# Kernel optimization log

Measured on AMD Instinct MI355X. Metric: run time of the kernel, lower is better.

## Reference

```python
import jax, jax.numpy as jnp
import numpy as np

B_TRUE, S, HEADS, DIM_HEAD, DIM, N = 2, 2, 8, 64, 512, 1024
BS = B_TRUE * S            # effective batch = (b s)
DIM_INNER = HEADS * DIM_HEAD
ALL_HEADS = S * HEADS
EPS = 1e-5


def setup_inputs() -> dict:
    key = jax.random.key(0)
    ks = jax.random.split(key, 8)
    inv = 0.02
    x = jax.random.normal(ks[0], (BS, N, DIM), dtype=jnp.float32)
    mask = jax.random.randint(ks[1], (BS, N), 0, 2).astype(bool)
    gamma = jnp.ones((DIM,), dtype=jnp.float32)
    w_qkv = jax.random.normal(ks[2], (3 * DIM_INNER, DIM), dtype=jnp.float32) * inv
    w_gates = jax.random.normal(ks[3], (HEADS, DIM), dtype=jnp.float32) * inv
    b_gates = jnp.zeros((HEADS,), dtype=jnp.float32)
    w_pre = jax.random.normal(ks[4], (ALL_HEADS, ALL_HEADS), dtype=jnp.float32) * 0.25
    w_post = jax.random.normal(ks[5], (ALL_HEADS, ALL_HEADS), dtype=jnp.float32) * 0.25
    w_out = jax.random.normal(ks[6], (DIM, DIM_INNER), dtype=jnp.float32) * inv
    return {"x": x, "mask": mask, "gamma": gamma, "w_qkv": w_qkv,
            "w_gates": w_gates, "b_gates": b_gates, "w_pre": w_pre,
            "w_post": w_post, "w_out": w_out}


def _rmsnorm(x, gamma):
    # einn.Norm('b... [d]', mean=False, bias=False): RMSNorm over last dim
    var = jnp.mean(jnp.square(x), axis=-1, keepdims=True)
    return x * jax.lax.rsqrt(var + EPS) * gamma


def reference(x, mask, gamma, w_qkv, w_gates, b_gates, w_pre, w_post, w_out):
    bs, n, dim = x.shape
    b = bs // S
    x = _rmsnorm(x, gamma)

    # QKV: 'b n (qkv h d) -> qkv b h n d'
    qkv = jnp.einsum('bnd,ed->bne', x, w_qkv)
    qkv = qkv.reshape(bs, n, 3, HEADS, DIM_HEAD).transpose(2, 0, 3, 1, 4)
    q, k, v = qkv[0], qkv[1], qkv[2]
    q = q * (DIM_HEAD ** 0.5)  # NOTE: source MULTIPLIES by sqrt(dim_head)

    sim = jnp.einsum('bhid,bhjd->bhij', q, k)  # [bs, h, n, n]
    mask_value = -jnp.finfo(sim.dtype).max

    # pre talking-heads: 1x1 conv across (s h) channels
    sim = sim.reshape(b, ALL_HEADS, n, n)
    sim = jnp.einsum('oi,binm->bonm', w_pre, sim).reshape(bs, HEADS, n, n)

    # padding mask over keys j
    sim = jnp.where(mask[:, None, None, :], sim, mask_value)

    # causal mask
    causal = jnp.triu(jnp.ones((n, n), dtype=bool), 1)
    sim = jnp.where(causal, mask_value, sim)

    attn = jax.nn.softmax(sim, axis=-1)
    post_softmax_attn = attn

    # post talking-heads
    attn = attn.reshape(b, ALL_HEADS, n, n)
    attn = jnp.einsum('oi,binm->bonm', w_post, attn).reshape(bs, HEADS, n, n)

    out = jnp.einsum('bhij,bhjd->bhid', attn, v)  # [bs, h, n, d]

    # sigmoid gates from normed x: 'b n h -> b h n 1'
    gates = jax.nn.sigmoid(jnp.einsum('bnd,hd->bnh', x, w_gates) + b_gates)
    out = out * gates.transpose(0, 2, 1)[..., None]

    # 'b h n d -> b n (h d)' then Linear(dim_inner, dim, bias=False)
    out = out.transpose(0, 2, 1, 3).reshape(bs, n, DIM_INNER)
    out = jnp.einsum('bne,de->bnd', out, w_out)
    return (out, post_softmax_attn)
```

## Files before the change

kernel.cpp:

```cpp
#include <hip/hip_runtime.h>
#include <cfloat>
#include <math.h>

#define B2   2
#define BS4  4
#define NH   8
#define DH   64
#define DIM  512
#define NSEQ 1024
#define AH   16

typedef __attribute__((ext_vector_type(8))) short short8;
typedef __attribute__((ext_vector_type(4))) float floatx4;

__device__ inline unsigned short f2bf(float x) {
    unsigned int u = __float_as_uint(x);
    unsigned int r = (u + 0x7fffu + ((u >> 16) & 1u)) >> 16;
    return (unsigned short)r;
}
__device__ inline float bf2f(unsigned short h) {
    return __uint_as_float(((unsigned int)h) << 16);
}
__device__ inline void split2(float x, unsigned short& h, unsigned short& l) {
    h = f2bf(x);
    l = f2bf(x - bf2f(h));
}

template<int MT, int NT_, bool SPLIT>
__device__ inline void mfma_nt_core(
    const unsigned short* __restrict__ Ah, const unsigned short* __restrict__ Al,
    const unsigned short* __restrict__ Bh, const unsigned short* __restrict__ Bl,
    int K, int lda, int ldb, int arow, int bcol, floatx4 acc[MT][NT_])
{
    int lane = threadIdx.x & 63;
    int lr = lane & 15, lq = lane >> 4;
    for (int k0 = 0; k0 < K; k0 += 32) {
        short8 ah[MT], al[MT], bh[NT_], bl[NT_];
        #pragma unroll
        for (int mi = 0; mi < MT; ++mi) {
            size_t off = (size_t)(arow + mi * 16 + lr) * lda + k0 + lq * 8;
            ah[mi] = *(const short8*)(Ah + off);
            if (SPLIT) al[mi] = *(const short8*)(Al + off);
        }
        #pragma unroll
        for (int ni = 0; ni < NT_; ++ni) {
            size_t off = (size_t)(bcol + ni * 16 + lr) * ldb + k0 + lq * 8;
            bh[ni] = *(const short8*)(Bh + off);
            if (SPLIT) bl[ni] = *(const short8*)(Bl + off);
        }
        #pragma unroll
        for (int mi = 0; mi < MT; ++mi)
            #pragma unroll
            for (int ni = 0; ni < NT_; ++ni) {
                acc[mi][ni] = __builtin_amdgcn_mfma_f32_16x16x32_bf16(ah[mi], bh[ni], acc[mi][ni], 0, 0, 0);
                if (SPLIT) {
                    acc[mi][ni] = __builtin_amdgcn_mfma_f32_16x16x32_bf16(ah[mi], bl[ni], acc[mi][ni], 0, 0, 0);
                    acc[mi][ni] = __builtin_amdgcn_mfma_f32_16x16x32_bf16(al[mi], bh[ni], acc[mi][ni], 0, 0, 0);
                }
            }
    }
}

__global__ __launch_bounds__(256) void k_rmsnorm_gates(
    const float* __restrict__ x, const float* __restrict__ gamma,
    const float* __restrict__ wg, const float* __restrict__ bg,
    unsigned short* __restrict__ xn_h, unsigned short* __restrict__ xn_l,
    float* __restrict__ gates)
{
    int r = blockIdx.x;
    int tid = threadIdx.x;
    const float* xr = x + (size_t)r * DIM;
    float v0 = xr[tid];
    float v1 = xr[tid + 256];
    float ss = v0 * v0 + v1 * v1;
    #pragma unroll
    for (int off = 32; off > 0; off >>= 1) ss += __shfl_down(ss, off, 64);
    __shared__ float sc[4];
    __shared__ float scw[NH][4];
    if ((tid & 63) == 0) sc[tid >> 6] = ss;
    __syncthreads();
    float tot = sc[0] + sc[1] + sc[2] + sc[3];
    float rs = rsqrtf(tot * (1.0f / DIM) + 1e-5f);
    float n0 = v0 * rs * gamma[tid];
    float n1 = v1 * rs * gamma[tid + 256];
    unsigned short hh, ll;
    split2(n0, hh, ll);
    xn_h[(size_t)r * DIM + tid] = hh; xn_l[(size_t)r * DIM + tid] = ll;
    split2(n1, hh, ll);
    xn_h[(size_t)r * DIM + tid + 256] = hh; xn_l[(size_t)r * DIM + tid + 256] = ll;
    #pragma unroll
    for (int h = 0; h < NH; ++h) {
        float p = n0 * wg[h * DIM + tid] + n1 * wg[h * DIM + tid + 256];
        #pragma unroll
        for (int off = 32; off > 0; off >>= 1) p += __shfl_down(p, off, 64);
        if ((tid & 63) == 0) scw[h][tid >> 6] = p;
    }
    __syncthreads();
    if (tid < NH) {
        float g = scw[tid][0] + scw[tid][1] + scw[tid][2] + scw[tid][3] + bg[tid];
        gates[(size_t)r * NH + tid] = 1.0f / (1.0f + __expf(-g));
    }
}

#define NQKV (3 * DIM * NH * DH)
#define NOUT (DIM * NH * DH)
__global__ __launch_bounds__(256) void k_cvt(
    const float* __restrict__ wqkv, const float* __restrict__ wout,
    unsigned short* __restrict__ wq_h, unsigned short* __restrict__ wq_l,
    unsigned short* __restrict__ wout_b)
{
    for (int i = blockIdx.x * 256 + threadIdx.x; i < NQKV + NOUT; i += gridDim.x * 256) {
        if (i < NQKV) {
            unsigned short hh, ll;
            split2(wqkv[i], hh, ll);
            wq_h[i] = hh; wq_l[i] = ll;
        } else {
            wout_b[i - NQKV] = f2bf(wout[i - NQKV]);
        }
    }
}

__global__ __launch_bounds__(256) void k_qkv_mfma(
    const unsigned short* __restrict__ xn_h, const unsigned short* __restrict__ xn_l,
    const unsigned short* __restrict__ wq_h, const unsigned short* __restrict__ wq_l,
    unsigned short* __restrict__ q_h, unsigned short* __restrict__ q_l,
    unsigned short* __restrict__ k_h, unsigned short* __restrict__ k_l,
    unsigned short* __restrict__ vT_b)
{
    int w = threadIdx.x >> 6;
    int am = blockIdx.y * 128 + (w & 1) * 64;
    int bn = blockIdx.x * 64 + (w >> 1) * 32;
    floatx4 acc[4][2];
    #pragma unroll
    for (int mi = 0; mi < 4; ++mi)
        #pragma unroll
        for (int ni = 0; ni < 2; ++ni) acc[mi][ni] = (floatx4){0.f, 0.f, 0.f, 0.f};
    mfma_nt_core<4, 2, true>(xn_h, xn_l, wq_h, wq_l, DIM, DIM, DIM, am, bn, acc);
    int lane = threadIdx.x & 63, lr = lane & 15, lq = lane >> 4;
    #pragma unroll
    for (int mi = 0; mi < 4; ++mi)
        #pragma unroll
        for (int ni = 0; ni < 2; ++ni)
            #pragma unroll
            for (int r = 0; r < 4; ++r) {
                int row = am + mi * 16 + lq * 4 + r;
                int col = bn + ni * 16 + lr;
                float v = acc[mi][ni][r];
                int bs = row >> 10, npos = row & 1023;
                int which = col >> 9, h = (col >> 6) & 7, d = col & 63;
                int bh = bs * 8 + h;
                if (which == 0) {
                    v *= 8.0f;
                    size_t idx = ((size_t)bh * NSEQ + npos) * DH + d;
                    unsigned short hh, ll; split2(v, hh, ll);
                    q_h[idx] = hh; q_l[idx] = ll;
                } else if (which == 1) {
                    size_t idx = ((size_t)bh * NSEQ + npos) * DH + d;
                    unsigned short hh, ll; split2(v, hh, ll);
                    k_h[idx] = hh; k_l[idx] = ll;
                } else {
                    vT_b[((size_t)bh * DH + d) * NSEQ + npos] = f2bf(v);
                }
            }
}

__global__ __launch_bounds__(256) void k_qk_mfma(
    const unsigned short* __restrict__ q_h, const unsigned short* __restrict__ q_l,
    const unsigned short* __restrict__ k_h, const unsigned short* __restrict__ k_l,
    float* __restrict__ simio)
{
    int bh = blockIdx.z;
    int w = threadIdx.x >> 6;
    int am = blockIdx.y * 128 + (w & 1) * 64;
    int bn = blockIdx.x * 64 + (w >> 1) * 32;
    const unsigned short* Ah = q_h + (size_t)bh * NSEQ * DH;
    const unsigned short* Al = q_l + (size_t)bh * NSEQ * DH;
    const unsigned short* Bh = k_h + (size_t)bh * NSEQ * DH;
    const unsigned short* Bl = k_l + (size_t)bh * NSEQ * DH;
    floatx4 acc[4][2];
    #pragma unroll
    for (int mi = 0; mi < 4; ++mi)
        #pragma unroll
        for (int ni = 0; ni < 2; ++ni) acc[mi][ni] = (floatx4){0.f, 0.f, 0.f, 0.f};
    mfma_nt_core<4, 2, true>(Ah, Al, Bh, Bl, DH, DH, DH, am, bn, acc);
    float* C = simio + ((size_t)bh << 20);
    int lane = threadIdx.x & 63, lr = lane & 15, lq = lane >> 4;
    #pragma unroll
    for (int mi = 0; mi < 4; ++mi)
        #pragma unroll
        for (int ni = 0; ni < 2; ++ni)
            #pragma unroll
            for (int r = 0; r < 4; ++r) {
                int row = am + mi * 16 + lq * 4 + r;
                int col = bn + ni * 16 + lr;
                C[(size_t)row * NSEQ + col] = acc[mi][ni][r];
            }
}

__global__ __launch_bounds__(256) void k_talk_softmax(
    float* __restrict__ simio, const int* __restrict__ mask,
    const float* __restrict__ wpre, const float* __restrict__ wpost,
    unsigned short* __restrict__ attn2_b)
{
    const int i = blockIdx.x;
    const int b = blockIdx.y;
    const int tid = threadIdx.x;
    const int wid = tid >> 6, lane = tid & 63;
    const int j0 = tid << 2;
    const size_t cstride = (size_t)NSEQ * NSEQ;
    const size_t rbase = (size_t)(b * 16) * cstride + (size_t)i * NSEQ + j0;

    const int4 mi0 = *(const int4*)(mask + (size_t)(b * 2 + 0) * NSEQ + j0);
    const int4 mi1 = *(const int4*)(mask + (size_t)(b * 2 + 1) * NSEQ + j0);
    bool mb[2][4];
    mb[0][0] = (mi0.x != 0) && (j0 + 0 <= i);
    mb[0][1] = (mi0.y != 0) && (j0 + 1 <= i);
    mb[0][2] = (mi0.z != 0) && (j0 + 2 <= i);
    mb[0][3] = (mi0.w != 0) && (j0 + 3 <= i);
    mb[1][0] = (mi1.x != 0) && (j0 + 0 <= i);
    mb[1][1] = (mi1.y != 0) && (j0 + 1 <= i);
    mb[1][2] = (mi1.z != 0) && (j0 + 2 <= i);
    mb[1][3] = (mi1.w != 0) && (j0 + 3 <= i);

    float val[16][4];
    #pragma unroll
    for (int o = 0; o < 16; ++o) {
        val[o][0] = 0.f; val[o][1] = 0.f; val[o][2] = 0.f; val[o][3] = 0.f;
    }
    #pragma unroll
    for (int c = 0; c < 16; ++c) {
        float4 r = *(const float4*)(simio + rbase + (size_t)c * cstride);
        #pragma unroll
        for (int o = 0; o < 16; ++o) {
            float w = wpre[o * 16 + c];
            val[o][0] = fmaf(w, r.x, val[o][0]);
            val[o][1] = fmaf(w, r.y, val[o][1]);
            val[o][2] = fmaf(w, r.z, val[o][2]);
            val[o][3] = fmaf(w, r.w, val[o][3]);
        }
    }
    #pragma unroll
    for (int o = 0; o < 16; ++o) {
        const int s = o >> 3;
        #pragma unroll
        for (int u = 0; u < 4; ++u)
            if (!mb[s][u]) val[o][u] = -FLT_MAX;
    }

    __shared__ float red[16][4];
    __shared__ float finmx[16];
    __shared__ float fininv[16];

    #pragma unroll
    for (int o = 0; o < 16; ++o) {
        float m = fmaxf(fmaxf(val[o][0], val[o][1]), fmaxf(val[o][2], val[o][3]));
        #pragma unroll
        for (int off = 32; off > 0; off >>= 1) m = fmaxf(m, __shfl_xor(m, off, 64));
        if (lane == 0) red[o][wid] = m;
    }
    __syncthreads();
    if (tid < 16)
        finmx[tid] = fmaxf(fmaxf(red[tid][0], red[tid][1]), fmaxf(red[tid][2], red[tid][3]));
    __syncthreads();

    #pragma unroll
    for (int o = 0; o < 16; ++o) {
        float mx = finmx[o];
        val[o][0] = __expf(val[o][0] - mx);
        val[o][1] = __expf(val[o][1] - mx);
        val[o][2] = __expf(val[o][2] - mx);
        val[o][3] = __expf(val[o][3] - mx);
        float s = (val[o][0] + val[o][1]) + (val[o][2] + val[o][3]);
        #pragma unroll
        for (int off = 32; off > 0; off >>= 1) s += __shfl_xor(s, off, 64);
        if (lane == 0) red[o][wid] = s;
    }
    __syncthreads();
    if (tid < 16)
        fininv[tid] = 1.0f / (red[tid][0] + red[tid][1] + red[tid][2] + red[tid][3]);
    __syncthreads();

    #pragma unroll
    for (int o = 0; o < 16; ++o) {
        float inv = fininv[o];
        val[o][0] *= inv; val[o][1] *= inv; val[o][2] *= inv; val[o][3] *= inv;
        *(float4*)(simio + rbase + (size_t)o * cstride) =
            make_float4(val[o][0], val[o][1], val[o][2], val[o][3]);
    }

    #pragma unroll
    for (int o = 0; o < 16; ++o) {
        float a0 = 0.f, a1 = 0.f, a2 = 0.f, a3 = 0.f;
        #pragma unroll
        for (int c = 0; c < 16; ++c) {
            float w = wpost[o * 16 + c];
            a0 = fmaf(w, val[c][0], a0);
            a1 = fmaf(w, val[c][1], a1);
            a2 = fmaf(w, val[c][2], a2);
            a3 = fmaf(w, val[c][3], a3);
        }
        unsigned long long pk = (unsigned long long)f2bf(a0)
                              | ((unsigned long long)f2bf(a1) << 16)
                              | ((unsigned long long)f2bf(a2) << 32)
                              | ((unsigned long long)f2bf(a3) << 48);
        *(unsigned long long*)(attn2_b + rbase + (size_t)o * cstride) = pk;
    }
}

__global__ __launch_bounds__(256) void k_av_mfma(
    const unsigned short* __restrict__ attn2_b, const unsigned short* __restrict__ vT_b,
    const float* __restrict__ gates, unsigned short* __restrict__ gated_b)
{
    int bh = blockIdx.y;
    int bs = bh >> 3, h = bh & 7;
    int w = threadIdx.x >> 6;
    int am = blockIdx.x * 64 + (w & 1) * 32;
    int bn = (w >> 1) * 32;
    const unsigned short* Ah = attn2_b + ((size_t)bh << 20);
    const unsigned short* Bh = vT_b + (size_t)bh * DH * NSEQ;
    floatx4 acc[2][2];
    #pragma unroll
    for (int mi = 0; mi < 2; ++mi)
        #pragma unroll
        for (int ni = 0; ni < 2; ++ni) acc[mi][ni] = (floatx4){0.f, 0.f, 0.f, 0.f};
    mfma_nt_core<2, 2, false>(Ah, nullptr, Bh, nullptr, NSEQ, NSEQ, NSEQ, am, bn, acc);
    int lane = threadIdx.x & 63, lr = lane & 15, lq = lane >> 4;
    #pragma unroll
    for (int mi = 0; mi < 2; ++mi)
        #pragma unroll
        for (int ni = 0; ni < 2; ++ni)
            #pragma unroll
            for (int r = 0; r < 4; ++r) {
                int i = am + mi * 16 + lq * 4 + r;
                int d = bn + ni * 16 + lr;
                float g = gates[((size_t)bs * NSEQ + i) * NH + h];
                gated_b[((size_t)bs * NSEQ + i) * DIM + h * DH + d] = f2bf(acc[mi][ni][r] * g);
            }
}

__global__ __launch_bounds__(256) void k_out_mfma(
    const unsigned short* __restrict__ gated_b, const unsigned short* __restrict__ wout_b,
    float* __restrict__ out)
{
    int w = threadIdx.x >> 6;
    int am = blockIdx.y * 64 + (w & 1) * 32;
    int bn = blockIdx.x * 64 + (w >> 1) * 32;
    floatx4 acc[2][2];
    #pragma unroll
    for (int mi = 0; mi < 2; ++mi)
        #pragma unroll
        for (int ni = 0; ni < 2; ++ni) acc[mi][ni] = (floatx4){0.f, 0.f, 0.f, 0.f};
    mfma_nt_core<2, 2, false>(gated_b, nullptr, wout_b, nullptr, DIM, DIM, DIM, am, bn, acc);
    int lane = threadIdx.x & 63, lr = lane & 15, lq = lane >> 4;
    #pragma unroll
    for (int mi = 0; mi < 2; ++mi)
        #pragma unroll
        for (int ni = 0; ni < 2; ++ni)
            #pragma unroll
            for (int r = 0; r < 4; ++r) {
                int row = am + mi * 16 + lq * 4 + r;
                int col = bn + ni * 16 + lr;
                out[(size_t)row * DIM + col] = acc[mi][ni][r];
            }
}

extern "C" void kernel_launch(void* const* d_in, const int* in_sizes, int n_in,
                              void* d_out, int out_size, void* d_ws, size_t ws_size,
                              hipStream_t stream)
{
    (void)in_sizes; (void)n_in; (void)out_size; (void)ws_size;

    const float* x     = (const float*)d_in[0];
    const int*   mask  = (const int*)  d_in[1];
    const float* gamma = (const float*)d_in[2];
    const float* wqkv  = (const float*)d_in[3];
    const float* wg    = (const float*)d_in[4];
    const float* bg    = (const float*)d_in[5];
    const float* wpre  = (const float*)d_in[6];
    const float* wpost = (const float*)d_in[7];
    const float* wout  = (const float*)d_in[8];

    float* out      = (float*)d_out;
    float* attn_out = out + (size_t)BS4 * NSEQ * DIM;

    char* ws = (char*)d_ws;
    unsigned short* xn_h    = (unsigned short*)(ws);
    unsigned short* xn_l    = (unsigned short*)(ws + 4194304);
    unsigned short* wq_h    = (unsigned short*)(ws + 8388608);
    unsigned short* wq_l    = (unsigned short*)(ws + 9961472);
    unsigned short* wout_b  = (unsigned short*)(ws + 11534336);
    float*          gates   = (float*)         (ws + 12058624);
    unsigned short* q_h     = (unsigned short*)(ws + 12189696);
    unsigned short* q_l     = (unsigned short*)(ws + 16384000);
    unsigned short* k_h     = (unsigned short*)(ws + 20578304);
    unsigned short* k_l     = (unsigned short*)(ws + 24772608);
    unsigned short* vT_b    = (unsigned short*)(ws + 28966912);
    unsigned short* gated_b = (unsigned short*)(ws + 33161216);
    unsigned short* attn2_b = (unsigned short*)(ws + 37355520);

    k_rmsnorm_gates<<<dim3(BS4 * NSEQ), dim3(256), 0, stream>>>(x, gamma, wg, bg, xn_h, xn_l, gates);
    k_cvt<<<dim3(1024), dim3(256), 0, stream>>>(wqkv, wout, wq_h, wq_l, wout_b);
    k_qkv_mfma<<<dim3(24, 32), dim3(256), 0, stream>>>(xn_h, xn_l, wq_h, wq_l, q_h, q_l, k_h, k_l, vT_b);
    k_qk_mfma<<<dim3(16, 8, 32), dim3(256), 0, stream>>>(q_h, q_l, k_h, k_l, attn_out);
    k_talk_softmax<<<dim3(NSEQ, B2), dim3(256), 0, stream>>>(attn_out, mask, wpre, wpost, attn2_b);
    k_av_mfma<<<dim3(16, 32), dim3(256), 0, stream>>>(attn2_b, vT_b, gates, gated_b);
    k_out_mfma<<<dim3(8, 64), dim3(256), 0, stream>>>(gated_b, wout_b, out);
}
```

Measured before the change: 409.9 us.

## Split talking-heads softmax into separate stats and normalize kernels

Splits the fused talking-heads softmax into two kernels. A reduce kernel computes per-row max and inverse sum and writes them to scratch. A norm kernel recomputes the pre-mix, normalizes, writes probabilities with nontemporal stores, and applies the post-mix. This removes the block-level reductions and barriers from the writing kernel, but re-reads the full similarity tensor and adds one launch.

```diff
diff --git a/kernel.cpp b/kernel.cpp
--- a/kernel.cpp
+++ b/kernel.cpp
@@ -197,10 +197,10 @@
             }
 }
 
-__global__ __launch_bounds__(256) void k_talk_softmax(
-    float* __restrict__ simio, const int* __restrict__ mask,
-    const float* __restrict__ wpre, const float* __restrict__ wpost,
-    unsigned short* __restrict__ attn2_b)
+__global__ __launch_bounds__(256) void k_talk_reduce(
+    const float* __restrict__ simio, const int* __restrict__ mask,
+    const float* __restrict__ wpre,
+    float* __restrict__ mx_out, float* __restrict__ inv_out)
 {
     const int i = blockIdx.x;
     const int b = blockIdx.y;
@@ -249,7 +249,6 @@
 
     __shared__ float red[16][4];
     __shared__ float finmx[16];
-    __shared__ float fininv[16];
 
     #pragma unroll
     for (int o = 0; o < 16; ++o) {
@@ -266,26 +265,81 @@
     #pragma unroll
     for (int o = 0; o < 16; ++o) {
         float mx = finmx[o];
-        val[o][0] = __expf(val[o][0] - mx);
-        val[o][1] = __expf(val[o][1] - mx);
-        val[o][2] = __expf(val[o][2] - mx);
-        val[o][3] = __expf(val[o][3] - mx);
-        float s = (val[o][0] + val[o][1]) + (val[o][2] + val[o][3]);
+        float s = (__expf(val[o][0] - mx) + __expf(val[o][1] - mx))
+                + (__expf(val[o][2] - mx) + __expf(val[o][3] - mx));
         #pragma unroll
         for (int off = 32; off > 0; off >>= 1) s += __shfl_xor(s, off, 64);
         if (lane == 0) red[o][wid] = s;
     }
     __syncthreads();
-    if (tid < 16)
-        fininv[tid] = 1.0f / (red[tid][0] + red[tid][1] + red[tid][2] + red[tid][3]);
-    __syncthreads();
-
-    #pragma unroll
-    for (int o = 0; o < 16; ++o) {
-        float inv = fininv[o];
-        val[o][0] *= inv; val[o][1] *= inv; val[o][2] *= inv; val[o][3] *= inv;
-        *(float4*)(simio + rbase + (size_t)o * cstride) =
-            make_float4(val[o][0], val[o][1], val[o][2], val[o][3]);
+    if (tid < 16) {
+        size_t sidx = ((size_t)b * NSEQ + i) * 16 + tid;
+        mx_out[sidx] = finmx[tid];
+        inv_out[sidx] = 1.0f / (red[tid][0] + red[tid][1] + red[tid][2] + red[tid][3]);
+    }
+}
+
+__global__ __launch_bounds__(256) void k_talk_norm(
+    float* __restrict__ simio, const int* __restrict__ mask,
+    const float* __restrict__ wpre, const float* __restrict__ wpost,
+    const float* __restrict__ mx_in, const float* __restrict__ inv_in,
+    unsigned short* __restrict__ attn2_b)
+{
+    const int i = blockIdx.x;
+    const int b = blockIdx.y;
+    const int tid = threadIdx.x;
+    const int j0 = tid << 2;
+    const size_t cstride = (size_t)NSEQ * NSEQ;
+    const size_t rbase = (size_t)(b * 16) * cstride + (size_t)i * NSEQ + j0;
+
+    const int4 mi0 = *(const int4*)(mask + (size_t)(b * 2 + 0) * NSEQ + j0);
+    const int4 mi1 = *(const int4*)(mask + (size_t)(b * 2 + 1) * NSEQ + j0);
+    bool mb[2][4];
+    mb[0][0] = (mi0.x != 0) && (j0 + 0 <= i);
+    mb[0][1] = (mi0.y != 0) && (j0 + 1 <= i);
+    mb[0][2] = (mi0.z != 0) && (j0 + 2 <= i);
+    mb[0][3] = (mi0.w != 0) && (j0 + 3 <= i);
+    mb[1][0] = (mi1.x != 0) && (j0 + 0 <= i);
+    mb[1][1] = (mi1.y != 0) && (j0 + 1 <= i);
+    mb[1][2] = (mi1.z != 0) && (j0 + 2 <= i);
+    mb[1][3] = (mi1.w != 0) && (j0 + 3 <= i);
+
+    float val[16][4];
+    #pragma unroll
+    for (int o = 0; o < 16; ++o) {
+        val[o][0] = 0.f; val[o][1] = 0.f; val[o][2] = 0.f; val[o][3] = 0.f;
+    }
+    #pragma unroll
+    for (int c = 0; c < 16; ++c) {
+        float4 r = *(const float4*)(simio + rbase + (size_t)c * cstride);
+        #pragma unroll
+        for (int o = 0; o < 16; ++o) {
+            float w = wpre[o * 16 + c];
+            val[o][0] = fmaf(w, r.x, val[o][0]);
+            val[o][1] = fmaf(w, r.y, val[o][1]);
+            val[o][2] = fmaf(w, r.z, val[o][2]);
+            val[o][3] = fmaf(w, r.w, val[o][3]);
+        }
+    }
+    #pragma unroll
+    for (int o = 0; o < 16; ++o) {
+        const int s = o >> 3;
+        #pragma unroll
+        for (int u = 0; u < 4; ++u)
+            if (!mb[s][u]) val[o][u] = -FLT_MAX;
+    }
+
+    const size_t sidx = ((size_t)b * NSEQ + i) * 16;
+    #pragma unroll
+    for (int o = 0; o < 16; ++o) {
+        float mx = mx_in[sidx + o];
+        float inv = inv_in[sidx + o];
+        val[o][0] = __expf(val[o][0] - mx) * inv;
+        val[o][1] = __expf(val[o][1] - mx) * inv;
+        val[o][2] = __expf(val[o][2] - mx) * inv;
+        val[o][3] = __expf(val[o][3] - mx) * inv;
+        floatx4 st = {val[o][0], val[o][1], val[o][2], val[o][3]};
+        __builtin_nontemporal_store(st, (floatx4*)(simio + rbase + (size_t)o * cstride));
     }
 
     #pragma unroll
@@ -398,11 +452,15 @@
     unsigned short* gated_b = (unsigned short*)(ws + 33161216);
     unsigned short* attn2_b = (unsigned short*)(ws + 37355520);
 
+    float* mx_stats  = (float*)xn_h;
+    float* inv_stats = (float*)xn_l;
+
     k_rmsnorm_gates<<<dim3(BS4 * NSEQ), dim3(256), 0, stream>>>(x, gamma, wg, bg, xn_h, xn_l, gates);
     k_cvt<<<dim3(1024), dim3(256), 0, stream>>>(wqkv, wout, wq_h, wq_l, wout_b);
     k_qkv_mfma<<<dim3(24, 32), dim3(256), 0, stream>>>(xn_h, xn_l, wq_h, wq_l, q_h, q_l, k_h, k_l, vT_b);
     k_qk_mfma<<<dim3(16, 8, 32), dim3(256), 0, stream>>>(q_h, q_l, k_h, k_l, attn_out);
-    k_talk_softmax<<<dim3(NSEQ, B2), dim3(256), 0, stream>>>(attn_out, mask, wpre, wpost, attn2_b);
+    k_talk_reduce<<<dim3(NSEQ, B2), dim3(256), 0, stream>>>(attn_out, mask, wpre, mx_stats, inv_stats);
+    k_talk_norm<<<dim3(NSEQ, B2), dim3(256), 0, stream>>>(attn_out, mask, wpre, wpost, mx_stats, inv_stats, attn2_b);
     k_av_mfma<<<dim3(16, 32), dim3(256), 0, stream>>>(attn2_b, vT_b, gates, gated_b);
     k_out_mfma<<<dim3(8, 64), dim3(256), 0, stream>>>(gated_b, wout_b, out);
 }
```

After: 462.5 us. +12.8%, slower.

## Store raw scores in row-interleaved workspace and stream probabilities with nontemporal stores

Applied to the files above, without the earlier changes.

The QK kernel now writes raw scores into a workspace laid out as [b][row][channel][col], so each talking-heads block reads its 16 channels from one contiguous 64KB region instead of 16 strided 4MB planes. Post-softmax probabilities go straight to the output with nontemporal stores. The post-mixed bf16 attention is written in place over the same workspace row, and the AV kernel reads it with a 32768-element row stride. The aim is better locality and fewer cache conflicts in the softmax kernel. The cost is a larger fp32 workspace and a strided A-operand in AV, which relies on the bf16 write never overtaking unread fp32 data in the same row.

```diff
diff --git a/kernel.cpp b/kernel.cpp
--- a/kernel.cpp
+++ b/kernel.cpp
@@ -167,9 +167,11 @@
 __global__ __launch_bounds__(256) void k_qk_mfma(
     const unsigned short* __restrict__ q_h, const unsigned short* __restrict__ q_l,
     const unsigned short* __restrict__ k_h, const unsigned short* __restrict__ k_l,
-    float* __restrict__ simio)
+    float* __restrict__ sim_ws)
 {
     int bh = blockIdx.z;
+    int b_true = bh >> 4;
+    int c = ((bh >> 3) & 1) * 8 + (bh & 7);
     int w = threadIdx.x >> 6;
     int am = blockIdx.y * 128 + (w & 1) * 64;
     int bn = blockIdx.x * 64 + (w >> 1) * 32;
@@ -183,7 +185,6 @@
         #pragma unroll
         for (int ni = 0; ni < 2; ++ni) acc[mi][ni] = (floatx4){0.f, 0.f, 0.f, 0.f};
     mfma_nt_core<4, 2, true>(Ah, Al, Bh, Bl, DH, DH, DH, am, bn, acc);
-    float* C = simio + ((size_t)bh << 20);
     int lane = threadIdx.x & 63, lr = lane & 15, lq = lane >> 4;
     #pragma unroll
     for (int mi = 0; mi < 4; ++mi)
@@ -193,14 +194,14 @@
             for (int r = 0; r < 4; ++r) {
                 int row = am + mi * 16 + lq * 4 + r;
                 int col = bn + ni * 16 + lr;
-                C[(size_t)row * NSEQ + col] = acc[mi][ni][r];
+                sim_ws[((size_t)(b_true * NSEQ + row) * 16 + c) * NSEQ + col] = acc[mi][ni][r];
             }
 }
 
-__global__ __launch_bounds__(256) void k_talk_softmax(
-    float* __restrict__ simio, const int* __restrict__ mask,
+__global__ __launch_bounds__(256) void k_talk(
+    float* __restrict__ sim_ws, const int* __restrict__ mask,
     const float* __restrict__ wpre, const float* __restrict__ wpost,
-    unsigned short* __restrict__ attn2_b)
+    float* __restrict__ probs_out)
 {
     const int i = blockIdx.x;
     const int b = blockIdx.y;
@@ -208,7 +209,7 @@
     const int wid = tid >> 6, lane = tid & 63;
     const int j0 = tid << 2;
     const size_t cstride = (size_t)NSEQ * NSEQ;
-    const size_t rbase = (size_t)(b * 16) * cstride + (size_t)i * NSEQ + j0;
+    float* simrow = sim_ws + (size_t)(b * NSEQ + i) * (16 * NSEQ);
 
     const int4 mi0 = *(const int4*)(mask + (size_t)(b * 2 + 0) * NSEQ + j0);
     const int4 mi1 = *(const int4*)(mask + (size_t)(b * 2 + 1) * NSEQ + j0);
@@ -229,7 +230,7 @@
     }
     #pragma unroll
     for (int c = 0; c < 16; ++c) {
-        float4 r = *(const float4*)(simio + rbase + (size_t)c * cstride);
+        float4 r = *(const float4*)(simrow + c * NSEQ + j0);
         #pragma unroll
         for (int o = 0; o < 16; ++o) {
             float w = wpre[o * 16 + c];
@@ -284,10 +285,12 @@
     for (int o = 0; o < 16; ++o) {
         float inv = fininv[o];
         val[o][0] *= inv; val[o][1] *= inv; val[o][2] *= inv; val[o][3] *= inv;
-        *(float4*)(simio + rbase + (size_t)o * cstride) =
-            make_float4(val[o][0], val[o][1], val[o][2], val[o][3]);
-    }
-
+        floatx4 st = {val[o][0], val[o][1], val[o][2], val[o][3]};
+        __builtin_nontemporal_store(st,
+            (floatx4*)(probs_out + (size_t)(b * 16 + o) * cstride + (size_t)i * NSEQ + j0));
+    }
+
+    unsigned short* a2row = (unsigned short*)simrow;
     #pragma unroll
     for (int o = 0; o < 16; ++o) {
         float a0 = 0.f, a1 = 0.f, a2 = 0.f, a3 = 0.f;
@@ -303,27 +306,29 @@
                               | ((unsigned long long)f2bf(a1) << 16)
                               | ((unsigned long long)f2bf(a2) << 32)
                               | ((unsigned long long)f2bf(a3) << 48);
-        *(unsigned long long*)(attn2_b + rbase + (size_t)o * cstride) = pk;
+        *(unsigned long long*)(a2row + o * NSEQ + j0) = pk;
     }
 }
 
 __global__ __launch_bounds__(256) void k_av_mfma(
-    const unsigned short* __restrict__ attn2_b, const unsigned short* __restrict__ vT_b,
+    const unsigned short* __restrict__ attn2_il, const unsigned short* __restrict__ vT_b,
     const float* __restrict__ gates, unsigned short* __restrict__ gated_b)
 {
     int bh = blockIdx.y;
     int bs = bh >> 3, h = bh & 7;
+    int b_true = bh >> 4;
+    int c = ((bh >> 3) & 1) * 8 + (bh & 7);
     int w = threadIdx.x >> 6;
     int am = blockIdx.x * 64 + (w & 1) * 32;
     int bn = (w >> 1) * 32;
-    const unsigned short* Ah = attn2_b + ((size_t)bh << 20);
+    const unsigned short* Ah = attn2_il + (size_t)b_true * NSEQ * 32768 + (size_t)c * NSEQ;
     const unsigned short* Bh = vT_b + (size_t)bh * DH * NSEQ;
     floatx4 acc[2][2];
     #pragma unroll
     for (int mi = 0; mi < 2; ++mi)
         #pragma unroll
         for (int ni = 0; ni < 2; ++ni) acc[mi][ni] = (floatx4){0.f, 0.f, 0.f, 0.f};
-    mfma_nt_core<2, 2, false>(Ah, nullptr, Bh, nullptr, NSEQ, NSEQ, NSEQ, am, bn, acc);
+    mfma_nt_core<2, 2, false>(Ah, nullptr, Bh, nullptr, NSEQ, 32768, NSEQ, am, bn, acc);
     int lane = threadIdx.x & 63, lr = lane & 15, lq = lane >> 4;
     #pragma unroll
     for (int mi = 0; mi < 2; ++mi)
@@ -380,8 +385,8 @@
     const float* wpost = (const float*)d_in[7];
     const float* wout  = (const float*)d_in[8];
 
-    float* out      = (float*)d_out;
-    float* attn_out = out + (size_t)BS4 * NSEQ * DIM;
+    float* out       = (float*)d_out;
+    float* probs_out = out + (size_t)BS4 * NSEQ * DIM;
 
     char* ws = (char*)d_ws;
     unsigned short* xn_h    = (unsigned short*)(ws);
@@ -396,13 +401,13 @@
     unsigned short* k_l     = (unsigned short*)(ws + 24772608);
     unsigned short* vT_b    = (unsigned short*)(ws + 28966912);
     unsigned short* gated_b = (unsigned short*)(ws + 33161216);
-    unsigned short* attn2_b = (unsigned short*)(ws + 37355520);
+    float*          sim_ws  = (float*)         (ws + 37355520);
 
     k_rmsnorm_gates<<<dim3(BS4 * NSEQ), dim3(256), 0, stream>>>(x, gamma, wg, bg, xn_h, xn_l, gates);
     k_cvt<<<dim3(1024), dim3(256), 0, stream>>>(wqkv, wout, wq_h, wq_l, wout_b);
     k_qkv_mfma<<<dim3(24, 32), dim3(256), 0, stream>>>(xn_h, xn_l, wq_h, wq_l, q_h, q_l, k_h, k_l, vT_b);
-    k_qk_mfma<<<dim3(16, 8, 32), dim3(256), 0, stream>>>(q_h, q_l, k_h, k_l, attn_out);
-    k_talk_softmax<<<dim3(NSEQ, B2), dim3(256), 0, stream>>>(attn_out, mask, wpre, wpost, attn2_b);
-    k_av_mfma<<<dim3(16, 32), dim3(256), 0, stream>>>(attn2_b, vT_b, gates, gated_b);
+    k_qk_mfma<<<dim3(16, 8, 32), dim3(256), 0, stream>>>(q_h, q_l, k_h, k_l, sim_ws);
+    k_talk<<<dim3(NSEQ, B2), dim3(256), 0, stream>>>(sim_ws, mask, wpre, wpost, probs_out);
+    k_av_mfma<<<dim3(16, 32), dim3(256), 0, stream>>>((unsigned short*)sim_ws, vT_b, gates, gated_b);
     k_out_mfma<<<dim3(8, 64), dim3(256), 0, stream>>>(gated_b, wout_b, out);
 }
```

Result: no change. 406.2 us (-0.9%).
